# Performance work log

Hardware: AMD Instinct MI355X
Metric: run time of the kernel (lower is better)

Reference implementation:

```python
import jax, jax.numpy as jnp
import numpy as np

B, P, ENC = 128, 196, 2048
A, E, D, V, L = 512, 512, 512, 10000, 52


def setup_inputs() -> dict:
    key = jax.random.key(0)
    ks = jax.random.split(key, 20)
    encoder_out = jax.random.normal(ks[0], (B, P, ENC), jnp.float32)
    encoded_captions = jax.random.randint(ks[1], (B, L), 0, V)
    lengths = jax.random.randint(ks[2], (B, 1), 20, L + 1)
    lengths = lengths.at[0, 0].set(L)  # guarantee max(decode_lengths) == L-1
    s = 0.05
    return {
        "encoder_out": encoder_out,
        "encoded_captions": encoded_captions,
        "caption_lengths": lengths,
        "emb": jax.random.uniform(ks[3], (V, E), jnp.float32, -0.1, 0.1),
        "We": jax.random.normal(ks[4], (A, ENC)) * s,   # attention.encoder_att
        "be": jnp.zeros((A,), jnp.float32),
        "Wd": jax.random.normal(ks[5], (A, D)) * s,     # attention.decoder_att
        "bd": jnp.zeros((A,), jnp.float32),
        "wf": jax.random.normal(ks[6], (1, A)) * s,     # attention.full_att
        "bf": jnp.zeros((1,), jnp.float32),
        "W_ih": jax.random.normal(ks[7], (4 * D, E + ENC)) * s,
        "b_ih": jnp.zeros((4 * D,), jnp.float32),
        "W_hh": jax.random.normal(ks[8], (4 * D, D)) * s,
        "b_hh": jnp.zeros((4 * D,), jnp.float32),
        "Wbeta": jax.random.normal(ks[9], (ENC, D)) * s,  # f_beta
        "bbeta": jnp.zeros((ENC,), jnp.float32),
        "Wfc": jax.random.uniform(ks[10], (V, D), jnp.float32, -0.1, 0.1),
        "bfc": jnp.zeros((V,), jnp.float32),
    }


def reference(encoder_out, encoded_captions, caption_lengths, emb, We, be, Wd, bd,
              wf, bf, W_ih, b_ih, W_hh, b_hh, Wbeta, bbeta, Wfc, bfc):
    lengths = caption_lengths[:, 0]
    order = jnp.argsort(-lengths)                 # sort descending by length
    lengths = lengths[order]
    enc = encoder_out[order]                      # (B,P,ENC)
    caps = encoded_captions[order]                # (B,L)
    dec_len = lengths - 1                         # decode_lengths
    T = caps.shape[1] - 1                         # max(decode_lengths), static

    embs = emb[caps[:, :T]]                       # (B,T,E)
    embs_t = jnp.transpose(embs, (1, 0, 2))       # (T,B,E)
    active_t = jnp.arange(T)[:, None] < dec_len[None, :]  # (T,B)

    enc_att = jnp.einsum('bpe,ae->bpa', enc, We) + be     # precompute encoder proj
    h0 = jnp.zeros((enc.shape[0], D), enc.dtype)
    c0 = jnp.zeros_like(h0)

    def step(carry, xs):
        h, c = carry
        emb_tok, active = xs                      # (B,E), (B,)
        dec_att = h @ Wd.T + bd                   # (B,A)
        att = jax.nn.relu(enc_att + dec_att[:, None, :])   # (B,P,A)
        scores = jnp.einsum('bpa,a->bp', att, wf[0]) + bf[0]
        alpha = jax.nn.softmax(scores, axis=-1)   # (B,P)
        awe = jnp.einsum('bp,bpe->be', alpha, enc)         # (B,ENC)
        gate = jax.nn.sigmoid(h @ Wbeta.T + bbeta)
        awe = gate * awe
        x = jnp.concatenate([emb_tok, awe], axis=1)        # (B,E+ENC)
        gates = x @ W_ih.T + b_ih + h @ W_hh.T + b_hh      # (B,4D)
        i, f, g, o = jnp.split(gates, 4, axis=1)
        c_new = jax.nn.sigmoid(f) * c + jax.nn.sigmoid(i) * jnp.tanh(g)
        h_new = jax.nn.sigmoid(o) * jnp.tanh(c_new)
        # rows past their decode length keep old state (matches shrinking-batch loop)
        m = active[:, None]
        h = jnp.where(m, h_new, h)
        c = jnp.where(m, c_new, c)
        preds = h_new @ Wfc.T + bfc               # dropout is identity in eval
        preds = jnp.where(m, preds, 0.0)
        return (h, c), preds

    _, preds_t = jax.lax.scan(step, (h0, c0), (embs_t, active_t))
    predictions = jnp.transpose(preds_t, (1, 0, 2))  # (B,T,V)
    return predictions, caps, dec_len
```

## Files before the change

kernel.cpp:

```cpp
#include <hip/hip_runtime.h>
#include <cstdint>
#include <cstddef>

#define B_ 128
#define P_ 196
#define ENC_ 2048
#define A_ 512
#define E_ 512
#define D_ 512
#define V_ 10000
#define L_ 52
#define T_ 51
#define ZPRE 8
#define ZG 8

using short8 = __attribute__((ext_vector_type(8))) short;
using short4v = __attribute__((ext_vector_type(4))) short;
using floatx4 = __attribute__((ext_vector_type(4))) float;

__device__ __forceinline__ float sigf(float x){ return 1.f/(1.f+expf(-x)); }

__device__ __forceinline__ unsigned short f2bf(float f){
  unsigned int u = __float_as_uint(f);
  unsigned int r = (u + 0x7fffu + ((u >> 16) & 1u)) >> 16;
  return (unsigned short)r;
}
__device__ __forceinline__ float bf2f(unsigned short u){
  return __uint_as_float(((unsigned int)u) << 16);
}

__global__ void sort_kernel(const int* __restrict__ cap_len, const int* __restrict__ caps,
                            int* __restrict__ order, int* __restrict__ dec_len,
                            int* __restrict__ caps_sorted,
                            float* __restrict__ out_caps, float* __restrict__ out_declen){
  __shared__ int len_s[B_];
  int i = threadIdx.x;
  len_s[i] = cap_len[i];
  __syncthreads();
  int li = len_s[i];
  int pos = 0;
  for (int j = 0; j < B_; j++){
    int lj = len_s[j];
    pos += (lj > li) || (lj == li && j < i);
  }
  order[pos] = i;
  dec_len[pos] = li - 1;
  out_declen[pos] = (float)(li - 1);
  for (int l = 0; l < L_; l++){
    int v = caps[i * L_ + l];
    caps_sorted[pos * L_ + l] = v;
    out_caps[pos * L_ + l] = (float)v;
  }
}

__global__ void gather_kernel(const float* __restrict__ enc, const int* __restrict__ order,
                              unsigned short* __restrict__ enc_s){
  int b = blockIdx.y;
  int i = (blockIdx.x * 256 + threadIdx.x) * 4;
  const float4 v = *(const float4*)(enc + (size_t)order[b] * (P_ * ENC_) + i);
  short4v r;
  r[0] = (short)f2bf(v.x); r[1] = (short)f2bf(v.y);
  r[2] = (short)f2bf(v.z); r[3] = (short)f2bf(v.w);
  *(short4v*)(enc_s + (size_t)b * (P_ * ENC_) + i) = r;
}

__global__ void prep_kernel(const float* __restrict__ We, const float* __restrict__ Wd,
                            const float* __restrict__ Wbeta,
                            const float* __restrict__ W_ih, const float* __restrict__ W_hh,
                            const float* __restrict__ Wfc,
                            const float* __restrict__ bd, const float* __restrict__ bbeta,
                            const float* __restrict__ b_ih, const float* __restrict__ b_hh,
                            unsigned short* __restrict__ We_b, unsigned short* __restrict__ Wpre_b,
                            unsigned short* __restrict__ Wg_b, unsigned short* __restrict__ Wfc_b,
                            float* __restrict__ bias_pre, float* __restrict__ bias_g,
                            float* __restrict__ h, float* __restrict__ c,
                            unsigned short* __restrict__ h_b, unsigned short* __restrict__ xh){
  unsigned int idx = blockIdx.x * blockDim.x + threadIdx.x;
  unsigned int stride = gridDim.x * blockDim.x;
  for (unsigned int i = idx; i < 512u * 2048u; i += stride) We_b[i] = f2bf(We[i]);
  for (unsigned int i = idx; i < 2560u * 512u; i += stride)
    Wpre_b[i] = f2bf(i < 512u * 512u ? Wd[i] : Wbeta[i - 512u * 512u]);
  for (unsigned int i = idx; i < 2048u * 3072u; i += stride){
    unsigned int j = i / 3072u, k = i - j * 3072u;
    Wg_b[i] = f2bf(k < 2560u ? W_ih[j * 2560u + k] : W_hh[j * 512u + (k - 2560u)]);
  }
  for (unsigned int i = idx; i < 10000u * 512u; i += stride) Wfc_b[i] = f2bf(Wfc[i]);
  for (unsigned int i = idx; i < 2560u; i += stride) bias_pre[i] = (i < 512u) ? bd[i] : bbeta[i - 512u];
  for (unsigned int i = idx; i < 2048u; i += stride) bias_g[i] = b_ih[i] + b_hh[i];
  for (unsigned int i = idx; i < (unsigned)B_ * D_; i += stride){
    h[i] = 0.f; c[i] = 0.f; h_b[i] = 0;
    unsigned int b = i >> 9, d = i & 511u;
    xh[(size_t)b * 3072 + 2560 + d] = 0;
  }
}

#define GEMM_CORE(Aptr, LDA, Bptr, LDB, KDIM, NCLAMP)                         \
  int tid = threadIdx.x; int lane = tid & 63; int w = tid >> 6;               \
  const floatx4 vzero = {0.f,0.f,0.f,0.f};                                    \
  floatx4 acc[4][4];                                                          \
  _Pragma("unroll") for (int i_=0;i_<4;i_++)                                  \
  _Pragma("unroll") for (int j_=0;j_<4;j_++) acc[i_][j_]=vzero;               \
  int mbase=(w&1)<<6, nbase=(w>>1)<<6;                                        \
  int fr=lane&15, fk=(lane>>4)<<3;                                            \
  for (int k0=0;k0<(KDIM);k0+=32){                                            \
    _Pragma("unroll") for (int r_=0;r_<2;r_++){                               \
      int chunk=r_*256+tid; int row=chunk>>2, kc=(chunk&3)<<3;                \
      short8 av=*(const short8*)((Aptr)+(size_t)(m0+row)*(LDA)+k0+kc);        \
      int bn=n0+row; if(bn>(NCLAMP)) bn=(NCLAMP);                             \
      short8 bv=*(const short8*)((Bptr)+(size_t)bn*(LDB)+k0+kc);              \
      *(short8*)&As[chunk*8]=av; *(short8*)&Bs[chunk*8]=bv; }                 \
    __syncthreads();                                                          \
    short8 af[4], bfrag[4];                                                   \
    _Pragma("unroll") for (int i_=0;i_<4;i_++){                               \
      af[i_]=*(const short8*)&As[(mbase+i_*16+fr)*32+fk];                     \
      bfrag[i_]=*(const short8*)&Bs[(nbase+i_*16+fr)*32+fk]; }                \
    _Pragma("unroll") for (int mi_=0;mi_<4;mi_++)                             \
    _Pragma("unroll") for (int ni_=0;ni_<4;ni_++)                             \
      acc[mi_][ni_]=__builtin_amdgcn_mfma_f32_16x16x32_bf16(af[mi_],bfrag[ni_],acc[mi_][ni_],0,0,0); \
    __syncthreads(); }

__launch_bounds__(256)
__global__ void gemm_bf16(const unsigned short* __restrict__ A, int lda,
                          const unsigned short* __restrict__ Bm, int ldb,
                          const float* __restrict__ bias,
                          float* __restrict__ Cf, unsigned short* __restrict__ Cb, int ldc,
                          int N, int ksz, int epi)
{
  __shared__ unsigned short As[128 * 32];
  __shared__ unsigned short Bs[128 * 32];
  int m0 = blockIdx.y * 128, n0 = blockIdx.x * 128;
  int kb = blockIdx.z * ksz;
  const unsigned short* Ap = A + kb;
  const unsigned short* Bp = Bm + kb;
  GEMM_CORE(Ap, lda, Bp, ldb, ksz, N - 1)
  float* Cz = Cf + (size_t)blockIdx.z * ((size_t)B_ * ldc);
#pragma unroll
  for (int mi = 0; mi < 4; mi++)
#pragma unroll
    for (int ni = 0; ni < 4; ni++){
      floatx4 v = acc[mi][ni];
      int col = n0 + nbase + ni * 16 + fr;
      int rb = m0 + mbase + mi * 16 + ((lane >> 4) << 2);
      if (epi == 0){
#pragma unroll
        for (int r = 0; r < 4; r++)
          Cz[(size_t)(rb + r) * ldc + col] = v[r];
      } else {
        float bb = bias[col];
#pragma unroll
        for (int r = 0; r < 4; r++)
          Cb[(size_t)(rb + r) * ldc + col] = f2bf(v[r] + bb);
      }
    }
}

__launch_bounds__(1024)
__global__ void attn_kernel(const unsigned short* __restrict__ enc_att,
                            const unsigned short* __restrict__ enc_s,
                            const float* __restrict__ ppart,
                            const float* __restrict__ bias_pre,
                            const float* __restrict__ wf, const float* __restrict__ bfp,
                            const float* __restrict__ emb, const int* __restrict__ caps_sorted,
                            unsigned short* __restrict__ xh,
                            int t){
  __shared__ float sc[P_];
  __shared__ float al[P_];
  __shared__ float red[256];
  __shared__ float part2[8][128][8];
  int b = blockIdx.y, bx = blockIdx.x, tid = threadIdx.x;

  int wid = tid >> 6, lane = tid & 63;
  float dav[8], wfv[8];
  {
    const float* bp = bias_pre + lane * 8;
    const float* p0 = ppart + (size_t)b * 2560 + lane * 8;
#pragma unroll
    for (int j = 0; j < 8; j++){
      float s = bp[j];
#pragma unroll
      for (int z = 0; z < ZPRE; z++) s += p0[(size_t)z * (B_ * 2560) + j];
      dav[j] = s;
    }
    *(float4*)&wfv[0] = *(const float4*)(wf + lane * 8);
    *(float4*)&wfv[4] = *(const float4*)(wf + lane * 8 + 4);
  }
  float bfv = bfp[0];
  for (int p = wid; p < P_; p += 16){
    short8 e = *(const short8*)(enc_att + ((size_t)b * P_ + p) * A_ + lane * 8);
    float s = 0.f;
#pragma unroll
    for (int j = 0; j < 8; j++){
      float v = bf2f((unsigned short)e[j]) + dav[j];
      s += fmaxf(v, 0.f) * wfv[j];
    }
#pragma unroll
    for (int off = 32; off > 0; off >>= 1) s += __shfl_down(s, off);
    if (lane == 0) sc[p] = s + bfv;
  }
  __syncthreads();

  if (tid < 256) red[tid] = (tid < P_) ? sc[tid] : -1e30f;
  __syncthreads();
  for (int s = 128; s > 0; s >>= 1){ if (tid < s) red[tid] = fmaxf(red[tid], red[tid + s]); __syncthreads(); }
  float mx = red[0];
  __syncthreads();
  float ex = 0.f;
  if (tid < 256){ ex = (tid < P_) ? expf(sc[tid] - mx) : 0.f; red[tid] = ex; }
  __syncthreads();
  for (int s = 128; s > 0; s >>= 1){ if (tid < s) red[tid] += red[tid + s]; __syncthreads(); }
  float inv = 1.f / red[0];
  if (tid < P_) al[tid] = ex * inv;
  __syncthreads();

  int pg = tid >> 7, et = tid & 127;
  int e0 = bx * 1024 + et * 8;
  const unsigned short* encb = enc_s + (size_t)b * (P_ * ENC_) + e0;
  float aa[8];
#pragma unroll
  for (int j = 0; j < 8; j++) aa[j] = 0.f;
  int pbeg = (pg * 196) >> 3, pend = ((pg + 1) * 196) >> 3;
#pragma unroll 5
  for (int p = pbeg; p < pend; p++){
    float a = al[p];
    short8 v = *(const short8*)(encb + (size_t)p * ENC_);
#pragma unroll
    for (int j = 0; j < 8; j++)
      aa[j] += a * bf2f((unsigned short)v[j]);
  }
#pragma unroll
  for (int j = 0; j < 8; j++) part2[pg][et][j] = aa[j];
  __syncthreads();
  if (pg == 0){
    float s[8];
#pragma unroll
    for (int j = 0; j < 8; j++){
      float acc = 0.f;
#pragma unroll
      for (int g = 0; g < 8; g++) acc += part2[g][et][j];
      s[j] = acc;
    }
    const float* bp = bias_pre + 512 + e0;
    const float* p0 = ppart + (size_t)b * 2560 + 512 + e0;
    short8 r;
#pragma unroll
    for (int j = 0; j < 8; j++){
      float g = bp[j];
#pragma unroll
      for (int z = 0; z < ZPRE; z++) g += p0[(size_t)z * (B_ * 2560) + j];
      r[j] = (short)f2bf(sigf(g) * s[j]);
    }
    *(short8*)(xh + (size_t)b * 3072 + 512 + e0) = r;
  }
  if (bx == 1 && tid < 512){
    int tok = caps_sorted[b * L_ + t];
    xh[(size_t)b * 3072 + tid] = f2bf(emb[(size_t)tok * E_ + tid]);
  }
}

__global__ void lstm_kernel(const float* __restrict__ gpart,
                            const float* __restrict__ bias_g,
                            float* __restrict__ h, float* __restrict__ c,
                            unsigned short* __restrict__ h_b, unsigned short* __restrict__ xh,
                            unsigned short* __restrict__ hnew_b,
                            const int* __restrict__ dec_len, int t){
  int idx = blockIdx.x * 256 + threadIdx.x;
  int b = idx >> 9, d = idx & 511;
  const float* gr = gpart + (size_t)b * 2048;
  float i_ = bias_g[d], f_ = bias_g[512 + d], g_ = bias_g[1024 + d], o_ = bias_g[1536 + d];
#pragma unroll
  for (int z = 0; z < ZG; z++){
    const float* gz = gr + (size_t)z * (B_ * 2048);
    i_ += gz[d]; f_ += gz[512 + d]; g_ += gz[1024 + d]; o_ += gz[1536 + d];
  }
  float cn = sigf(f_) * c[idx] + sigf(i_) * tanhf(g_);
  float hn = sigf(o_) * tanhf(cn);
  bool act = t < dec_len[b];
  float hv = act ? hn : h[idx];
  float cv = act ? cn : c[idx];
  h[idx] = hv; c[idx] = cv;
  unsigned short hvb = f2bf(hv);
  h_b[idx] = hvb;
  xh[(size_t)b * 3072 + 2560 + d] = hvb;
  hnew_b[(size_t)t * (B_ * D_) + idx] = f2bf(hn);
}

__launch_bounds__(256)
__global__ void gemm_preds(const unsigned short* __restrict__ A,
                           const unsigned short* __restrict__ Bm,
                           const float* __restrict__ bias,
                           float* __restrict__ Cf,
                           const int* __restrict__ dec_len){
  __shared__ __attribute__((aligned(16))) char smem[4 * 64 * 68 * 4];
  unsigned short* As = (unsigned short*)smem;
  unsigned short* Bs = (unsigned short*)(smem + 8192);
  int bid = blockIdx.x;
  int xcd = bid & 7, i = bid >> 3;
  int mchunk = xcd >> 1, nchunk = xcd & 1;
  int mi_ = i % 13, ni_ = i / 13;
  int mt = mchunk * 13 + mi_;
  int nt = nchunk * 40 + ni_;
  if (mt >= 51 || nt >= 79) return;
  int m0 = mt * 128, n0 = nt * 128;
  GEMM_CORE(A, D_, Bm, D_, D_, V_ - 1)
  float* Cs = (float*)smem + (size_t)w * (64 * 68);
#pragma unroll
  for (int mi = 0; mi < 4; mi++)
#pragma unroll
    for (int ni = 0; ni < 4; ni++){
      int lc = ni * 16 + fr;
      int col = n0 + nbase + lc;
      float bb = bias[col < V_ ? col : V_ - 1];
#pragma unroll
      for (int r = 0; r < 4; r++){
        int lr = mi * 16 + ((lane >> 4) << 2) + r;
        Cs[lr * 68 + lc] = acc[mi][ni][r] + bb;
      }
    }
#pragma unroll
  for (int rd = 0; rd < 16; rd++){
    int lr = rd * 4 + (lane >> 4);
    int m = m0 + mbase + lr;
    int tt = m >> 7, b = m & 127;
    int col = n0 + nbase + fr * 4;
    floatx4 v = *(const floatx4*)&Cs[lr * 68 + fr * 4];
    if (tt >= dec_len[b]){ v[0] = 0.f; v[1] = 0.f; v[2] = 0.f; v[3] = 0.f; }
    if (col < V_)
      __builtin_nontemporal_store(v, (floatx4*)(Cf + ((size_t)b * T_ + tt) * V_ + col));
  }
}

extern "C" void kernel_launch(void* const* d_in, const int* in_sizes, int n_in,
                              void* d_out, int out_size, void* d_ws, size_t ws_size,
                              hipStream_t stream) {
  const float* encoder_out = (const float*)d_in[0];
  const int*   caps        = (const int*)d_in[1];
  const int*   cap_len     = (const int*)d_in[2];
  const float* emb         = (const float*)d_in[3];
  const float* We          = (const float*)d_in[4];
  const float* be          = (const float*)d_in[5];
  const float* Wd          = (const float*)d_in[6];
  const float* bd          = (const float*)d_in[7];
  const float* wf          = (const float*)d_in[8];
  const float* bf          = (const float*)d_in[9];
  const float* W_ih        = (const float*)d_in[10];
  const float* b_ih        = (const float*)d_in[11];
  const float* W_hh        = (const float*)d_in[12];
  const float* b_hh        = (const float*)d_in[13];
  const float* Wbeta       = (const float*)d_in[14];
  const float* bbeta       = (const float*)d_in[15];
  const float* Wfc         = (const float*)d_in[16];
  const float* bfc         = (const float*)d_in[17];

  float* out_preds  = (float*)d_out;
  float* out_caps   = out_preds + (size_t)B_ * T_ * V_;
  float* out_declen = out_caps + (size_t)B_ * L_;

  char* w = (char*)d_ws;
  auto alloc = [&](size_t bytes) -> void* {
    void* p = (void*)w;
    w += (bytes + 255) & ~(size_t)255;
    return p;
  };
  int*   order       = (int*)alloc(B_ * 4);
  int*   dec_len     = (int*)alloc(B_ * 4);
  int*   caps_sorted = (int*)alloc((size_t)B_ * L_ * 4);
  unsigned short* enc_s   = (unsigned short*)alloc((size_t)B_ * P_ * ENC_ * 2);
  unsigned short* We_b    = (unsigned short*)alloc((size_t)512 * 2048 * 2);
  unsigned short* Wpre_b  = (unsigned short*)alloc((size_t)2560 * 512 * 2);
  unsigned short* Wg_b    = (unsigned short*)alloc((size_t)2048 * 3072 * 2);
  unsigned short* Wfc_b   = (unsigned short*)alloc((size_t)10000 * 512 * 2);
  unsigned short* enc_att = (unsigned short*)alloc((size_t)B_ * P_ * A_ * 2);
  float* bias_pre    = (float*)alloc(2560 * 4);
  float* bias_g      = (float*)alloc(2048 * 4);
  float* ppart       = (float*)alloc((size_t)ZPRE * B_ * 2560 * 4);
  float* gpart       = (float*)alloc((size_t)ZG * B_ * 2048 * 4);
  unsigned short* xh = (unsigned short*)alloc((size_t)B_ * 3072 * 2);
  float* h           = (float*)alloc((size_t)B_ * D_ * 4);
  float* c           = (float*)alloc((size_t)B_ * D_ * 4);
  unsigned short* h_b = (unsigned short*)alloc((size_t)B_ * D_ * 2);
  unsigned short* hnew_b = (unsigned short*)alloc((size_t)T_ * B_ * D_ * 2);

  sort_kernel<<<1, 128, 0, stream>>>(cap_len, caps, order, dec_len, caps_sorted, out_caps, out_declen);
  gather_kernel<<<dim3(392, 128), 256, 0, stream>>>(encoder_out, order, enc_s);
  prep_kernel<<<2048, 256, 0, stream>>>(We, Wd, Wbeta, W_ih, W_hh, Wfc, bd, bbeta, b_ih, b_hh,
                                        We_b, Wpre_b, Wg_b, Wfc_b, bias_pre, bias_g,
                                        h, c, h_b, xh);

  gemm_bf16<<<dim3(4, 196, 1), 256, 0, stream>>>(
      enc_s, ENC_, We_b, ENC_, be, nullptr, enc_att, A_, A_, ENC_, 1);

  for (int t = 0; t < T_; t++){
    gemm_bf16<<<dim3(20, 1, ZPRE), 256, 0, stream>>>(
        h_b, D_, Wpre_b, D_, nullptr, ppart, nullptr, 2560, 2560, 512 / ZPRE, 0);

    attn_kernel<<<dim3(2, B_), 1024, 0, stream>>>(enc_att, enc_s, ppart, bias_pre, wf, bf,
                                                  emb, caps_sorted, xh, t);

    gemm_bf16<<<dim3(16, 1, ZG), 256, 0, stream>>>(
        xh, 3072, Wg_b, 3072, nullptr, gpart, nullptr, 2048, 2048, 3072 / ZG, 0);

    lstm_kernel<<<(B_ * D_) / 256, 256, 0, stream>>>(gpart, bias_g, h, c, h_b, xh, hnew_b,
                                                     dec_len, t);
  }

  gemm_preds<<<4160, 256, 0, stream>>>(hnew_b, Wfc_b, bfc, out_preds, dec_len);
}
```

Before: 3.394 ms.

## Use one attention block per batch row so scores are not recomputed

The attention kernel previously ran two blocks per batch row, and each block recomputed the full score and softmax over all positions just to handle half of the encoder columns. Now one block per row computes the scores once, and each thread accumulates 16 encoder columns across a fixed 25-position slice. A zeroed padding region after enc_s and zero-filled alpha entries cover the reads past position 196. The cost is half as many blocks (128) in flight and more registers per thread.

```diff
diff --git a/kernel.cpp b/kernel.cpp
--- a/kernel.cpp
+++ b/kernel.cpp
@@ -74,9 +74,11 @@
                             unsigned short* __restrict__ Wg_b, unsigned short* __restrict__ Wfc_b,
                             float* __restrict__ bias_pre, float* __restrict__ bias_g,
                             float* __restrict__ h, float* __restrict__ c,
-                            unsigned short* __restrict__ h_b, unsigned short* __restrict__ xh){
+                            unsigned short* __restrict__ h_b, unsigned short* __restrict__ xh,
+                            unsigned short* __restrict__ enc_pad){
   unsigned int idx = blockIdx.x * blockDim.x + threadIdx.x;
   unsigned int stride = gridDim.x * blockDim.x;
+  for (unsigned int i = idx; i < 8192u; i += stride) enc_pad[i] = 0;
   for (unsigned int i = idx; i < 512u * 2048u; i += stride) We_b[i] = f2bf(We[i]);
   for (unsigned int i = idx; i < 2560u * 512u; i += stride)
     Wpre_b[i] = f2bf(i < 512u * 512u ? Wd[i] : Wbeta[i - 512u * 512u]);
@@ -164,10 +166,10 @@
                             unsigned short* __restrict__ xh,
                             int t){
   __shared__ float sc[P_];
-  __shared__ float al[P_];
+  __shared__ float al[200];
   __shared__ float red[256];
-  __shared__ float part2[8][128][8];
-  int b = blockIdx.y, bx = blockIdx.x, tid = threadIdx.x;
+  __shared__ float part2[8][128][16];
+  int b = blockIdx.x, tid = threadIdx.x;
 
   int wid = tid >> 6, lane = tid & 63;
   float dav[8], wfv[8];
@@ -210,30 +212,34 @@
   for (int s = 128; s > 0; s >>= 1){ if (tid < s) red[tid] += red[tid + s]; __syncthreads(); }
   float inv = 1.f / red[0];
   if (tid < P_) al[tid] = ex * inv;
+  else if (tid < 200) al[tid] = 0.f;
   __syncthreads();
 
   int pg = tid >> 7, et = tid & 127;
-  int e0 = bx * 1024 + et * 8;
-  const unsigned short* encb = enc_s + (size_t)b * (P_ * ENC_) + e0;
-  float aa[8];
-#pragma unroll
-  for (int j = 0; j < 8; j++) aa[j] = 0.f;
-  int pbeg = (pg * 196) >> 3, pend = ((pg + 1) * 196) >> 3;
+  int e0 = et * 16;
+  const unsigned short* encb = enc_s + (size_t)b * (P_ * ENC_) + (size_t)(pg * 25) * ENC_ + e0;
+  const float* alp = al + pg * 25;
+  float aa[16];
+#pragma unroll
+  for (int j = 0; j < 16; j++) aa[j] = 0.f;
 #pragma unroll 5
-  for (int p = pbeg; p < pend; p++){
-    float a = al[p];
-    short8 v = *(const short8*)(encb + (size_t)p * ENC_);
-#pragma unroll
-    for (int j = 0; j < 8; j++)
-      aa[j] += a * bf2f((unsigned short)v[j]);
-  }
-#pragma unroll
-  for (int j = 0; j < 8; j++) part2[pg][et][j] = aa[j];
+  for (int p = 0; p < 25; p++){
+    float a = alp[p];
+    short8 v0 = *(const short8*)(encb + (size_t)p * ENC_);
+    short8 v1 = *(const short8*)(encb + (size_t)p * ENC_ + 8);
+#pragma unroll
+    for (int j = 0; j < 8; j++){
+      aa[j]     += a * bf2f((unsigned short)v0[j]);
+      aa[8 + j] += a * bf2f((unsigned short)v1[j]);
+    }
+  }
+#pragma unroll
+  for (int j = 0; j < 16; j++) part2[pg][et][j] = aa[j];
   __syncthreads();
   if (pg == 0){
-    float s[8];
-#pragma unroll
-    for (int j = 0; j < 8; j++){
+    float s[16];
+#pragma unroll
+    for (int j = 0; j < 16; j++){
       float acc = 0.f;
 #pragma unroll
       for (int g = 0; g < 8; g++) acc += part2[g][et][j];
@@ -241,17 +247,20 @@
     }
     const float* bp = bias_pre + 512 + e0;
     const float* p0 = ppart + (size_t)b * 2560 + 512 + e0;
-    short8 r;
-#pragma unroll
-    for (int j = 0; j < 8; j++){
+    short8 r0, r1;
+#pragma unroll
+    for (int j = 0; j < 16; j++){
       float g = bp[j];
 #pragma unroll
       for (int z = 0; z < ZPRE; z++) g += p0[(size_t)z * (B_ * 2560) + j];
-      r[j] = (short)f2bf(sigf(g) * s[j]);
-    }
-    *(short8*)(xh + (size_t)b * 3072 + 512 + e0) = r;
-  }
-  if (bx == 1 && tid < 512){
+      float val = sigf(g) * s[j];
+      if (j < 8) r0[j] = (short)f2bf(val);
+      else       r1[j - 8] = (short)f2bf(val);
+    }
+    *(short8*)(xh + (size_t)b * 3072 + 512 + e0) = r0;
+    *(short8*)(xh + (size_t)b * 3072 + 512 + e0 + 8) = r1;
+  }
+  if (tid < 512){
     int tok = caps_sorted[b * L_ + t];
     xh[(size_t)b * 3072 + tid] = f2bf(emb[(size_t)tok * E_ + tid]);
   }
@@ -364,7 +373,7 @@
   int*   order       = (int*)alloc(B_ * 4);
   int*   dec_len     = (int*)alloc(B_ * 4);
   int*   caps_sorted = (int*)alloc((size_t)B_ * L_ * 4);
-  unsigned short* enc_s   = (unsigned short*)alloc((size_t)B_ * P_ * ENC_ * 2);
+  unsigned short* enc_s   = (unsigned short*)alloc((size_t)B_ * P_ * ENC_ * 2 + 16384);
   unsigned short* We_b    = (unsigned short*)alloc((size_t)512 * 2048 * 2);
   unsigned short* Wpre_b  = (unsigned short*)alloc((size_t)2560 * 512 * 2);
   unsigned short* Wg_b    = (unsigned short*)alloc((size_t)2048 * 3072 * 2);
@@ -384,7 +393,8 @@
   gather_kernel<<<dim3(392, 128), 256, 0, stream>>>(encoder_out, order, enc_s);
   prep_kernel<<<2048, 256, 0, stream>>>(We, Wd, Wbeta, W_ih, W_hh, Wfc, bd, bbeta, b_ih, b_hh,
                                         We_b, Wpre_b, Wg_b, Wfc_b, bias_pre, bias_g,
-                                        h, c, h_b, xh);
+                                        h, c, h_b, xh,
+                                        enc_s + (size_t)B_ * P_ * ENC_);
 
   gemm_bf16<<<dim3(4, 196, 1), 256, 0, stream>>>(
       enc_s, ENC_, We_b, ENC_, be, nullptr, enc_att, A_, A_, ENC_, 1);
@@ -393,8 +403,8 @@
     gemm_bf16<<<dim3(20, 1, ZPRE), 256, 0, stream>>>(
         h_b, D_, Wpre_b, D_, nullptr, ppart, nullptr, 2560, 2560, 512 / ZPRE, 0);
 
-    attn_kernel<<<dim3(2, B_), 1024, 0, stream>>>(enc_att, enc_s, ppart, bias_pre, wf, bf,
-                                                  emb, caps_sorted, xh, t);
+    attn_kernel<<<B_, 1024, 0, stream>>>(enc_att, enc_s, ppart, bias_pre, wf, bf,
+                                         emb, caps_sorted, xh, t);
 
     gemm_bf16<<<dim3(16, 1, ZG), 256, 0, stream>>>(
         xh, 3072, Wg_b, 3072, nullptr, gpart, nullptr, 2048, 2048, 3072 / ZG, 0);
```

Measured after the change: 3.493 ms. +2.9%, slower.
